# Optimization experiments

Measured on AMD Instinct MI355X. Metric: run time of the kernel, lower is better.

Reference implementation:

```python
import jax, jax.numpy as jnp
import numpy as np

BN_EPS = 1e-5


def conv1x1(x, w, b):
    # x: [B,C,H,W], w: [O,C] (squeezed 1x1 kernel), b: [O]
    return jnp.einsum('bchw,oc->bohw', x, w) + b[None, :, None, None]


def setup_inputs() -> dict:
    key = jax.random.key(0)
    ks = jax.random.split(key, 12)
    B, C, H, W = 4, 64, 256, 256
    s = 1.0 / np.sqrt(C).astype(np.float32)
    inp = {
        'x': jax.random.normal(ks[0], (B, C, H, W), jnp.float32),
        'theta_w': jax.random.normal(ks[1], (C, C), jnp.float32) * s,
        'theta_b': jax.random.normal(ks[2], (C,), jnp.float32) * 0.01,
        'phi_w': jax.random.normal(ks[3], (C, C), jnp.float32) * s,
        'phi_b': jax.random.normal(ks[4], (C,), jnp.float32) * 0.01,
        'g_w': jax.random.normal(ks[5], (C, C), jnp.float32) * s,
        'g_b': jax.random.normal(ks[6], (C,), jnp.float32) * 0.01,
        'w_w': jax.random.normal(ks[7], (C, C), jnp.float32) * s,
        'w_b': jax.random.normal(ks[8], (C,), jnp.float32) * 0.01,
        'bn_gamma': jax.random.normal(ks[9], (C,), jnp.float32) * 0.1,
        'bn_beta': jax.random.normal(ks[10], (C,), jnp.float32) * 0.1,
    }
    return inp


def reference(x, theta_w, theta_b, phi_w, phi_b, g_w, g_b, w_w, w_b, bn_gamma, bn_beta):
    B, C, H, W = x.shape
    N = H * W
    g_x = conv1x1(x, g_w, g_b).reshape(B, C, N)          # [B,C,N]
    theta_x = conv1x1(x, theta_w, theta_b).reshape(B, C, N)
    phi_x = conv1x1(x, phi_w, phi_b).reshape(B, C, N)
    # f = phi_x @ theta_x^T : channel-channel affinity [B,C,C]
    f = jnp.einsum('bcn,bdn->bcd', phi_x, theta_x)
    attn = jax.nn.softmax(f, axis=-1)                    # [B,C,C]
    y = jnp.einsum('bcd,bdn->bcn', attn, g_x)            # [B,C,N]
    # faithful to torch: permute(0,2,1).contiguous().view(B,C,H,W)
    y = jnp.transpose(y, (0, 2, 1)).reshape(B, C, H, W)
    w_y = conv1x1(y, w_w, w_b)                           # [B,C,H,W]
    # BatchNorm2d in training mode: batch stats over (B,H,W), biased var
    mean = jnp.mean(w_y, axis=(0, 2, 3), keepdims=True)
    var = jnp.var(w_y, axis=(0, 2, 3), keepdims=True)
    w_y = (w_y - mean) * jax.lax.rsqrt(var + BN_EPS)
    w_y = w_y * bn_gamma[None, :, None, None] + bn_beta[None, :, None, None]
    return w_y + x
```

## Files before the change

kernel.cpp:

```cpp
#include <hip/hip_runtime.h>
#include <hip/hip_bf16.h>
#include <stdint.h>

namespace {

constexpr size_t OFF_G     = 0;
constexpr size_t OFF_S     = 65536;
constexpr size_t OFF_M     = 66560;
constexpr size_t OFF_AB    = 132096;
constexpr size_t OFF_SCALE = 133120;
constexpr size_t OFF_STATS = 133632;
constexpr size_t OFF_WWT   = 134144;
constexpr size_t OFF_WSUM  = 150528;
constexpr size_t OFF_SPART = 150784;
constexpr size_t OFF_GPART = 412928;
constexpr size_t OFF_V     = 17190144;
constexpr size_t OFF_WY    = 50744576;

__device__ __forceinline__ float bf2f(unsigned short u) {
    return __uint_as_float(((unsigned)u) << 16);
}
__device__ __forceinline__ unsigned short f2bf(float f) {
    union { __hip_bfloat16 h; unsigned short u; } cv;
    cv.h = __float2bfloat16(f);
    return cv.u;
}

__global__ __launch_bounds__(256) void k_trans(const float* __restrict__ Ww,
                                               float* __restrict__ WwT,
                                               float* __restrict__ Wsum) {
    const int t = threadIdx.x;
    for (int e = t; e < 4096; e += 256) {
        const int o = e >> 6, c = e & 63;
        WwT[c * 64 + o] = Ww[e];
    }
    if (t < 64) {
        float s = 0.f;
#pragma unroll 8
        for (int c = 0; c < 64; ++c) s += Ww[t * 64 + c];
        Wsum[t] = s;
    }
}

__global__ __launch_bounds__(128) void k_gram(const float* __restrict__ x,
                                              float* __restrict__ gpart,
                                              float* __restrict__ spart) {
    const int wg = blockIdx.x;
    const int b = wg >> 8;
    const int chunk = wg & 255;
    const int t = threadIdx.x;
    const int wv = t >> 6;
    const int l = t & 63;
    const int g = l >> 3, h = l & 7;

    __shared__ __align__(16) float tile[64][64];
    __shared__ __align__(16) float Gred[4096];

    float acc[8][8];
#pragma unroll
    for (int i = 0; i < 8; ++i)
#pragma unroll
        for (int j = 0; j < 8; ++j) acc[i][j] = 0.f;
    float sp[8];
#pragma unroll
    for (int i = 0; i < 8; ++i) sp[i] = 0.f;

    const float* xb = x + (size_t)b * 64 * 65536 + chunk * 256;

    for (int t4 = 0; t4 < 4; ++t4) {
#pragma unroll
        for (int it = 0; it < 8; ++it) {
            const int v = it * 128 + t;
            const int row = v >> 4;
            const int c4 = v & 15;
            const float4 val = *(const float4*)(xb + (size_t)row * 65536 + t4 * 64 + c4 * 4);
            const int c4s = c4 ^ (row >> 3);
            *(float4*)&tile[row][c4s * 4] = val;
            sp[it] += val.x + val.y + val.z + val.w;
        }
        __syncthreads();
        const int fbase = wv * 8;
#pragma unroll
        for (int fs = 0; fs < 8; ++fs) {
            const int f = fbase + fs;
            float4 a4[8], b4[8];
#pragma unroll
            for (int i = 0; i < 8; ++i) a4[i] = *(const float4*)&tile[g * 8 + i][(f ^ g) * 4];
#pragma unroll
            for (int j = 0; j < 8; ++j) b4[j] = *(const float4*)&tile[h * 8 + j][(f ^ h) * 4];
#pragma unroll
            for (int i = 0; i < 8; ++i)
#pragma unroll
                for (int j = 0; j < 8; ++j) {
                    acc[i][j] += a4[i].x * b4[j].x;
                    acc[i][j] += a4[i].y * b4[j].y;
                    acc[i][j] += a4[i].z * b4[j].z;
                    acc[i][j] += a4[i].w * b4[j].w;
                }
        }
        __syncthreads();
    }

    if (wv == 1) {
#pragma unroll
        for (int i = 0; i < 8; ++i)
#pragma unroll
            for (int j4 = 0; j4 < 2; ++j4) {
                float4 v;
                v.x = acc[i][j4 * 4 + 0]; v.y = acc[i][j4 * 4 + 1];
                v.z = acc[i][j4 * 4 + 2]; v.w = acc[i][j4 * 4 + 3];
                *(float4*)&Gred[(g * 8 + i) * 64 + h * 8 + j4 * 4] = v;
            }
    }
    __syncthreads();
    if (wv == 0) {
        float* gp = gpart + (size_t)wg * 4096;
#pragma unroll
        for (int i = 0; i < 8; ++i)
#pragma unroll
            for (int j4 = 0; j4 < 2; ++j4) {
                const float4 r = *(const float4*)&Gred[(g * 8 + i) * 64 + h * 8 + j4 * 4];
                float4 v;
                v.x = acc[i][j4 * 4 + 0] + r.x; v.y = acc[i][j4 * 4 + 1] + r.y;
                v.z = acc[i][j4 * 4 + 2] + r.z; v.w = acc[i][j4 * 4 + 3] + r.w;
                *(float4*)(gp + (g * 8 + i) * 64 + h * 8 + j4 * 4) = v;
            }
    }
#pragma unroll
    for (int it = 0; it < 8; ++it) {
        float v = sp[it];
        v += __shfl_xor(v, 1);
        v += __shfl_xor(v, 2);
        v += __shfl_xor(v, 4);
        v += __shfl_xor(v, 8);
        if ((l & 15) == 0) {
            const int row = it * 8 + (t >> 4);
            spart[((size_t)b * 256 + chunk) * 64 + row] = v;
        }
    }
}

__global__ __launch_bounds__(256) void k_gred(const float* __restrict__ gpart,
                                              const float* __restrict__ spart,
                                              float* __restrict__ G,
                                              float* __restrict__ s) {
    const int b = blockIdx.x >> 4;
    const int part = blockIdx.x & 15;
    const int t = threadIdx.x;
    const int e4l = t & 63;
    const int cg = t >> 6;
    const int e4 = part * 64 + e4l;
    const float4* gp4 = (const float4*)gpart;

    float4 a = make_float4(0.f, 0.f, 0.f, 0.f);
#pragma unroll 8
    for (int i = 0; i < 64; ++i) {
        const int w = cg * 64 + i;
        const float4 v = gp4[((size_t)b * 256 + w) * 1024 + e4];
        a.x += v.x; a.y += v.y; a.z += v.z; a.w += v.w;
    }
    __shared__ __align__(16) float4 red[4][64];
    __shared__ float reds[4][64];
    red[cg][e4l] = a;

    float sv = 0.f;
    if (part == 0) {
#pragma unroll 8
        for (int i = 0; i < 64; ++i) {
            const int w = cg * 64 + i;
            sv += spart[((size_t)b * 256 + w) * 64 + e4l];
        }
        reds[cg][e4l] = sv;
    }
    __syncthreads();
    if (cg == 0) {
        const float4 r1 = red[1][e4l], r2 = red[2][e4l], r3 = red[3][e4l];
        float4 o;
        o.x = a.x + r1.x + r2.x + r3.x;
        o.y = a.y + r1.y + r2.y + r3.y;
        o.z = a.z + r1.z + r2.z + r3.z;
        o.w = a.w + r1.w + r2.w + r3.w;
        *(float4*)(G + (size_t)b * 4096 + (size_t)e4 * 4) = o;
        if (part == 0) {
            s[b * 64 + e4l] = sv + reds[1][e4l] + reds[2][e4l] + reds[3][e4l];
        }
    }
}

__global__ __launch_bounds__(256) void k_small(const float* __restrict__ G,
                                               const float* __restrict__ s,
                                               const float* __restrict__ Pw,
                                               const float* __restrict__ pb,
                                               const float* __restrict__ Tw,
                                               const float* __restrict__ tb,
                                               const float* __restrict__ Gw,
                                               const float* __restrict__ gb,
                                               float* __restrict__ M,
                                               float* __restrict__ ab) {
    const int b = blockIdx.x >> 1;
    const int rblk = (blockIdx.x & 1) * 32;
    const int t = threadIdx.x;
    const int rl = t >> 3;
    const int seg = t & 7;
    const int d0 = seg * 8;
    const int rg = rblk + rl;

    __shared__ __align__(16) float GL[64][68];
    __shared__ __align__(16) float TwL[64][68];
    __shared__ __align__(16) float GwL[64][68];
    __shared__ __align__(16) float PwL[32][68];
    __shared__ __align__(16) float AL[32][68];
    __shared__ __align__(16) float atL[32][68];
    __shared__ float sL[64], TsL[64], PsL[32], pbL[64], tbL[64], gbL[64];

    for (int v = t; v < 1024; v += 256) {
        const int k = v >> 4, c4 = (v & 15) * 4;
        *(float4*)&GL[k][c4]  = *(const float4*)(G + (size_t)b * 4096 + (size_t)v * 4);
        *(float4*)&TwL[k][c4] = *(const float4*)(Tw + (size_t)v * 4);
        *(float4*)&GwL[k][c4] = *(const float4*)(Gw + (size_t)v * 4);
    }
    for (int v = t; v < 512; v += 256) {
        const int k = v >> 4, c4 = (v & 15) * 4;
        *(float4*)&PwL[k][c4] = *(const float4*)(Pw + (size_t)(rblk + k) * 64 + c4);
    }
    if (t < 64) {
        sL[t] = s[b * 64 + t];
        pbL[t] = pb[t]; tbL[t] = tb[t]; gbL[t] = gb[t];
    }
    __syncthreads();
    if (t < 64) {
        float a = 0.f;
#pragma unroll 8
        for (int k = 0; k < 64; ++k) a += TwL[t][k] * sL[k];
        TsL[t] = a;
    }
    if (t < 32) {
        float a = 0.f;
#pragma unroll 8
        for (int k = 0; k < 64; ++k) a += PwL[t][k] * sL[k];
        PsL[t] = a;
    }
    {
        float4 a1 = make_float4(0.f, 0.f, 0.f, 0.f), a2 = make_float4(0.f, 0.f, 0.f, 0.f);
#pragma unroll 4
        for (int k = 0; k < 64; ++k) {
            const float pw = PwL[rl][k];
            const float4 g1 = *(const float4*)&GL[k][d0];
            const float4 g2 = *(const float4*)&GL[k][d0 + 4];
            a1.x += pw * g1.x; a1.y += pw * g1.y; a1.z += pw * g1.z; a1.w += pw * g1.w;
            a2.x += pw * g2.x; a2.y += pw * g2.y; a2.z += pw * g2.z; a2.w += pw * g2.w;
        }
        *(float4*)&AL[rl][d0] = a1;
        *(float4*)&AL[rl][d0 + 4] = a2;
    }
    __syncthreads();
    float4 areg[16];
#pragma unroll
    for (int i = 0; i < 16; ++i) areg[i] = *(const float4*)&AL[rl][i * 4];
    float fv[8];
#pragma unroll
    for (int dd = 0; dd < 8; ++dd) {
        const int d = d0 + dd;
        float4 a4 = make_float4(0.f, 0.f, 0.f, 0.f);
#pragma unroll
        for (int i = 0; i < 16; ++i) {
            const float4 tw = *(const float4*)&TwL[d][i * 4];
            a4.x += areg[i].x * tw.x; a4.y += areg[i].y * tw.y;
            a4.z += areg[i].z * tw.z; a4.w += areg[i].w * tw.w;
        }
        const float dot = (a4.x + a4.y) + (a4.z + a4.w);
        fv[dd] = dot + PsL[rl] * tbL[d] + pbL[rg] * (TsL[d] + 65536.f * tbL[d]);
    }
    float mx = fv[0];
#pragma unroll
    for (int dd = 1; dd < 8; ++dd) mx = fmaxf(mx, fv[dd]);
    mx = fmaxf(mx, __shfl_xor(mx, 1));
    mx = fmaxf(mx, __shfl_xor(mx, 2));
    mx = fmaxf(mx, __shfl_xor(mx, 4));
    float sm = 0.f;
#pragma unroll
    for (int dd = 0; dd < 8; ++dd) { fv[dd] = __expf(fv[dd] - mx); sm += fv[dd]; }
    sm += __shfl_xor(sm, 1);
    sm += __shfl_xor(sm, 2);
    sm += __shfl_xor(sm, 4);
    const float inv = 1.f / sm;
    float4 p1, p2;
    p1.x = fv[0] * inv; p1.y = fv[1] * inv; p1.z = fv[2] * inv; p1.w = fv[3] * inv;
    p2.x = fv[4] * inv; p2.y = fv[5] * inv; p2.z = fv[6] * inv; p2.w = fv[7] * inv;
    *(float4*)&atL[rl][d0] = p1;
    *(float4*)&atL[rl][d0 + 4] = p2;
    __syncthreads();
#pragma unroll
    for (int i = 0; i < 16; ++i) areg[i] = *(const float4*)&atL[rl][i * 4];
    float4 m1 = make_float4(0.f, 0.f, 0.f, 0.f), m2 = make_float4(0.f, 0.f, 0.f, 0.f);
    float abv = 0.f;
#pragma unroll
    for (int d4 = 0; d4 < 16; ++d4) {
        const float4 a = areg[d4];
#define MSTEP(comp, dc) { \
        const int d = d4 * 4 + dc; \
        const float ad = a.comp; \
        const float4 g1 = *(const float4*)&GwL[d][d0]; \
        const float4 g2 = *(const float4*)&GwL[d][d0 + 4]; \
        m1.x += ad * g1.x; m1.y += ad * g1.y; m1.z += ad * g1.z; m1.w += ad * g1.w; \
        m2.x += ad * g2.x; m2.y += ad * g2.y; m2.z += ad * g2.z; m2.w += ad * g2.w; \
        abv += ad * gbL[d]; }
        MSTEP(x, 0) MSTEP(y, 1) MSTEP(z, 2) MSTEP(w, 3)
#undef MSTEP
    }
    float* Mrow = M + ((size_t)b * 64 + rg) * 64;
    *(float4*)(Mrow + d0) = m1;
    *(float4*)(Mrow + d0 + 4) = m2;
    if (seg == 0) ab[b * 64 + rg] = abv;
}

__global__ __launch_bounds__(256) void k_convV(const float* __restrict__ x,
                                               const float* __restrict__ WwT,
                                               unsigned short* __restrict__ V) {
    const int bid = blockIdx.x;
    const int b = bid >> 8;
    const int k = (bid >> 2) & 63;
    const int qc = bid & 3;
    const int q = qc * 256 + threadIdx.x;
    const float* xr = x + ((size_t)b * 64 + k) * 65536 + q;
    float4 acc[16];
#pragma unroll
    for (int i = 0; i < 16; ++i) acc[i] = make_float4(0.f, 0.f, 0.f, 0.f);
#pragma unroll 2
    for (int cp = 0; cp < 64; ++cp) {
        const float xv = xr[(size_t)cp * 1024];
        const float4* wt = (const float4*)(WwT + cp * 64);
#pragma unroll
        for (int i = 0; i < 16; ++i) {
            const float4 w = wt[i];
            acc[i].x += w.x * xv; acc[i].y += w.y * xv;
            acc[i].z += w.z * xv; acc[i].w += w.w * xv;
        }
    }
    unsigned short* vp = V + (size_t)b * 64 * 65536 + (size_t)k * 1024 + q;
#pragma unroll
    for (int i = 0; i < 16; ++i) {
        vp[(size_t)(i * 4 + 0) * 65536] = f2bf(acc[i].x);
        vp[(size_t)(i * 4 + 1) * 65536] = f2bf(acc[i].y);
        vp[(size_t)(i * 4 + 2) * 65536] = f2bf(acc[i].z);
        vp[(size_t)(i * 4 + 3) * 65536] = f2bf(acc[i].w);
    }
}

__global__ __launch_bounds__(256) void k_wy(const unsigned short* __restrict__ V,
                                            const float* __restrict__ M,
                                            const float* __restrict__ ab,
                                            const float* __restrict__ Wsum,
                                            const float* __restrict__ wb,
                                            unsigned short* __restrict__ wy,
                                            float* __restrict__ stats) {
    const int bid = blockIdx.x;
    const int b = bid >> 9;
    const int o = (bid >> 3) & 63;
    const int qc = bid & 7;
    const int t = threadIdx.x;
    const int ql = t & 127;
    const int rh = __builtin_amdgcn_readfirstlane((t >> 7) * 32);
    const int q = qc * 128 + ql;

    const unsigned short* vsrc = V + ((size_t)b * 64 + o) * 65536 + q;
    float v[64];
#pragma unroll
    for (int k = 0; k < 64; ++k) v[k] = bf2f(vsrc[(size_t)k * 1024]);

    const float wsum_o = Wsum[o];
    const float wb_o = wb[o];
    const float* Mb = M + ((size_t)b * 64 + rh) * 64;
    const float* abb = ab + (size_t)b * 64 + rh;

    float ssum = 0.f, ssq = 0.f;
    unsigned pack[16];
#pragma unroll 4
    for (int ri = 0; ri < 32; ++ri) {
        const float4* mr4 = (const float4*)(Mb + ri * 64);
        float4 a4 = make_float4(0.f, 0.f, 0.f, 0.f);
#pragma unroll
        for (int i = 0; i < 16; ++i) {
            const float4 m = mr4[i];
            a4.x += m.x * v[i * 4 + 0];
            a4.y += m.y * v[i * 4 + 1];
            a4.z += m.z * v[i * 4 + 2];
            a4.w += m.w * v[i * 4 + 3];
        }
        const float val = (a4.x + a4.y) + (a4.z + a4.w) + wsum_o * abb[ri] + wb_o;
        ssum += val; ssq += val * val;
        const unsigned h = (unsigned)f2bf(val);
        if ((ri & 1) == 0) pack[ri >> 1] = h;
        else pack[ri >> 1] |= h << 16;
    }
    unsigned short* wp = wy + ((size_t)b * 64 + o) * 65536 + (size_t)q * 64 + rh;
#pragma unroll
    for (int i = 0; i < 4; ++i) {
        *(uint4*)(wp + i * 8) = make_uint4(pack[i * 4 + 0], pack[i * 4 + 1],
                                           pack[i * 4 + 2], pack[i * 4 + 3]);
    }
    float v1 = ssum, v2 = ssq;
#pragma unroll
    for (int off = 1; off < 64; off <<= 1) {
        v1 += __shfl_xor(v1, off);
        v2 += __shfl_xor(v2, off);
    }
    if ((t & 63) == 0) {
        atomicAdd(&stats[o], v1);
        atomicAdd(&stats[64 + o], v2);
    }
}

__global__ __launch_bounds__(64) void k_statfin(const float* __restrict__ stats,
                                                const float* __restrict__ gamma,
                                                const float* __restrict__ beta,
                                                float* __restrict__ scaleA,
                                                float* __restrict__ shiftB) {
    const int o = threadIdx.x;
    const float invn = 1.f / 262144.f;
    const float mean = stats[o] * invn;
    const float var = stats[64 + o] * invn - mean * mean;
    const float sA = gamma[o] * rsqrtf(var + 1e-5f);
    scaleA[o] = sA;
    shiftB[o] = beta[o] - mean * sA;
}

__global__ __launch_bounds__(256) void k_out(const unsigned short* __restrict__ wy,
                                             const float* __restrict__ x,
                                             const float* __restrict__ scaleA,
                                             const float* __restrict__ shiftB,
                                             float* __restrict__ out) {
    const size_t stride = (size_t)gridDim.x * blockDim.x;
    for (size_t i8 = (size_t)blockIdx.x * blockDim.x + threadIdx.x; i8 < 2097152; i8 += stride) {
        const size_t base = i8 * 8;
        const int o = (int)((base >> 16) & 63);
        const uint4 u = *(const uint4*)(wy + base);
        const float4 x1 = *(const float4*)(x + base);
        const float4 x2 = *(const float4*)(x + base + 4);
        const float a = scaleA[o];
        const float c = shiftB[o];
        float4 o1, o2;
        o1.x = __uint_as_float(u.x << 16) * a + c + x1.x;
        o1.y = __uint_as_float(u.x & 0xffff0000u) * a + c + x1.y;
        o1.z = __uint_as_float(u.y << 16) * a + c + x1.z;
        o1.w = __uint_as_float(u.y & 0xffff0000u) * a + c + x1.w;
        o2.x = __uint_as_float(u.z << 16) * a + c + x2.x;
        o2.y = __uint_as_float(u.z & 0xffff0000u) * a + c + x2.y;
        o2.z = __uint_as_float(u.w << 16) * a + c + x2.z;
        o2.w = __uint_as_float(u.w & 0xffff0000u) * a + c + x2.w;
        *(float4*)(out + base) = o1;
        *(float4*)(out + base + 4) = o2;
    }
}

}

extern "C" void kernel_launch(void* const* d_in, const int* in_sizes, int n_in,
                              void* d_out, int out_size, void* d_ws, size_t ws_size,
                              hipStream_t stream) {
    const float* x        = (const float*)d_in[0];
    const float* theta_w  = (const float*)d_in[1];
    const float* theta_b  = (const float*)d_in[2];
    const float* phi_w    = (const float*)d_in[3];
    const float* phi_b    = (const float*)d_in[4];
    const float* g_w      = (const float*)d_in[5];
    const float* g_b      = (const float*)d_in[6];
    const float* w_w      = (const float*)d_in[7];
    const float* w_b      = (const float*)d_in[8];
    const float* bn_gamma = (const float*)d_in[9];
    const float* bn_beta  = (const float*)d_in[10];
    float* out = (float*)d_out;
    char* ws = (char*)d_ws;

    float* G      = (float*)(ws + OFF_G);
    float* s      = (float*)(ws + OFF_S);
    float* M      = (float*)(ws + OFF_M);
    float* ab     = (float*)(ws + OFF_AB);
    float* scaleA = (float*)(ws + OFF_SCALE);
    float* shiftB = scaleA + 64;
    float* stats  = (float*)(ws + OFF_STATS);
    float* WwT    = (float*)(ws + OFF_WWT);
    float* Wsum   = (float*)(ws + OFF_WSUM);
    float* spart  = (float*)(ws + OFF_SPART);
    float* gpart  = (float*)(ws + OFF_GPART);
    unsigned short* V  = (unsigned short*)(ws + OFF_V);
    unsigned short* wy = (unsigned short*)(ws + OFF_WY);

    (void)in_sizes; (void)n_in; (void)out_size; (void)ws_size;

    hipMemsetAsync(stats, 0, 512, stream);
    hipLaunchKernelGGL(k_trans, dim3(1), dim3(256), 0, stream, w_w, WwT, Wsum);
    hipLaunchKernelGGL(k_gram, dim3(1024), dim3(128), 0, stream, x, gpart, spart);
    hipLaunchKernelGGL(k_gred, dim3(64), dim3(256), 0, stream, gpart, spart, G, s);
    hipLaunchKernelGGL(k_small, dim3(8), dim3(256), 0, stream, G, s, phi_w, phi_b,
                       theta_w, theta_b, g_w, g_b, M, ab);
    hipLaunchKernelGGL(k_convV, dim3(1024), dim3(256), 0, stream, x, WwT, V);
    hipLaunchKernelGGL(k_wy, dim3(2048), dim3(256), 0, stream, V, M, ab, Wsum, w_b, wy, stats);
    hipLaunchKernelGGL(k_statfin, dim3(1), dim3(64), 0, stream, stats, bn_gamma, bn_beta,
                       scaleA, shiftB);
    hipLaunchKernelGGL(k_out, dim3(2048), dim3(256), 0, stream, wy, x, scaleA, shiftB, out);
}
```

Measured before the change: 296.7 us.

## Register-tile convV and wy kernels as 16x8 outer products with vectorized bf16 I/O

Rewrites k_convV and k_wy so each thread computes a 16-output by 8-position register tile. Weights are broadcast per wave, and activations are loaded as float4/uint4 vectors instead of scalar strided loads. M is stored transposed so k_wy can read 16 contiguous rows per k. Output stores become packed 128-bit bf16 writes instead of scattered 16-bit stores. Grids halve or quarter and register pressure rises with 128 accumulators per thread, which may lower occupancy.

```diff
diff --git a/kernel.cpp b/kernel.cpp
--- a/kernel.cpp
+++ b/kernel.cpp
@@ -25,6 +25,9 @@
     cv.h = __float2bfloat16(f);
     return cv.u;
 }
+__device__ __forceinline__ unsigned pack2bf(float a, float b) {
+    return (unsigned)f2bf(a) | ((unsigned)f2bf(b) << 16);
+}
 
 __global__ __launch_bounds__(256) void k_trans(const float* __restrict__ Ww,
                                                float* __restrict__ WwT,
@@ -195,7 +198,7 @@
                                                const float* __restrict__ tb,
                                                const float* __restrict__ Gw,
                                                const float* __restrict__ gb,
-                                               float* __restrict__ M,
+                                               float* __restrict__ Mt,
                                                float* __restrict__ ab) {
     const int b = blockIdx.x >> 1;
     const int rblk = (blockIdx.x & 1) * 32;
@@ -308,9 +311,10 @@
         MSTEP(x, 0) MSTEP(y, 1) MSTEP(z, 2) MSTEP(w, 3)
 #undef MSTEP
     }
-    float* Mrow = M + ((size_t)b * 64 + rg) * 64;
-    *(float4*)(Mrow + d0) = m1;
-    *(float4*)(Mrow + d0 + 4) = m2;
+    float mv[8] = {m1.x, m1.y, m1.z, m1.w, m2.x, m2.y, m2.z, m2.w};
+    float* Mb = Mt + (size_t)b * 4096;
+#pragma unroll
+    for (int dd = 0; dd < 8; ++dd) Mb[(d0 + dd) * 64 + rg] = mv[dd];
     if (seg == 0) ab[b * 64 + rg] = abv;
 }
 
@@ -318,87 +322,134 @@
                                                const float* __restrict__ WwT,
                                                unsigned short* __restrict__ V) {
     const int bid = blockIdx.x;
-    const int b = bid >> 8;
-    const int k = (bid >> 2) & 63;
-    const int qc = bid & 3;
-    const int q = qc * 256 + threadIdx.x;
-    const float* xr = x + ((size_t)b * 64 + k) * 65536 + q;
-    float4 acc[16];
-#pragma unroll
-    for (int i = 0; i < 16; ++i) acc[i] = make_float4(0.f, 0.f, 0.f, 0.f);
-#pragma unroll 2
-    for (int cp = 0; cp < 64; ++cp) {
-        const float xv = xr[(size_t)cp * 1024];
-        const float4* wt = (const float4*)(WwT + cp * 64);
+    const int b = bid >> 7;
+    const int k = (bid >> 1) & 63;
+    const int qh = bid & 1;
+    const int t = threadIdx.x;
+    const int wv = __builtin_amdgcn_readfirstlane(t >> 6);
+    const int l = t & 63;
+    const int q0 = qh * 512 + l * 8;
+    const int o0 = wv * 16;
+
+    const float* xb = x + ((size_t)b * 64 + k) * 65536 + q0;
+    const float* wt = WwT + o0;
+
+    float acc[16][8];
+#pragma unroll
+    for (int i = 0; i < 16; ++i)
+#pragma unroll
+        for (int j = 0; j < 8; ++j) acc[i][j] = 0.f;
+
+    for (int c = 0; c < 64; ++c) {
+        const float4 x1 = *(const float4*)(xb + (size_t)c * 1024);
+        const float4 x2 = *(const float4*)(xb + (size_t)c * 1024 + 4);
+        const float xv[8] = {x1.x, x1.y, x1.z, x1.w, x2.x, x2.y, x2.z, x2.w};
+        const float4* wp = (const float4*)(wt + c * 64);
+        const float4 w0 = wp[0], w1 = wp[1], w2 = wp[2], w3 = wp[3];
+        const float wv16[16] = {w0.x, w0.y, w0.z, w0.w, w1.x, w1.y, w1.z, w1.w,
+                                w2.x, w2.y, w2.z, w2.w, w3.x, w3.y, w3.z, w3.w};
 #pragma unroll
         for (int i = 0; i < 16; ++i) {
-            const float4 w = wt[i];
-            acc[i].x += w.x * xv; acc[i].y += w.y * xv;
-            acc[i].z += w.z * xv; acc[i].w += w.w * xv;
-        }
-    }
-    unsigned short* vp = V + (size_t)b * 64 * 65536 + (size_t)k * 1024 + q;
+            const float w = wv16[i];
+#pragma unroll
+            for (int j = 0; j < 8; ++j) acc[i][j] += w * xv[j];
+        }
+    }
+    unsigned short* vb = V + (((size_t)b * 64 + o0) * 64 + k) * 1024 + q0;
 #pragma unroll
     for (int i = 0; i < 16; ++i) {
-        vp[(size_t)(i * 4 + 0) * 65536] = f2bf(acc[i].x);
-        vp[(size_t)(i * 4 + 1) * 65536] = f2bf(acc[i].y);
-        vp[(size_t)(i * 4 + 2) * 65536] = f2bf(acc[i].z);
-        vp[(size_t)(i * 4 + 3) * 65536] = f2bf(acc[i].w);
+        uint4 pk;
+        pk.x = pack2bf(acc[i][0], acc[i][1]);
+        pk.y = pack2bf(acc[i][2], acc[i][3]);
+        pk.z = pack2bf(acc[i][4], acc[i][5]);
+        pk.w = pack2bf(acc[i][6], acc[i][7]);
+        *(uint4*)(vb + (size_t)i * 65536) = pk;
     }
 }
 
 __global__ __launch_bounds__(256) void k_wy(const unsigned short* __restrict__ V,
-                                            const float* __restrict__ M,
+                                            const float* __restrict__ Mt,
                                             const float* __restrict__ ab,
                                             const float* __restrict__ Wsum,
                                             const float* __restrict__ wb,
                                             unsigned short* __restrict__ wy,
                                             float* __restrict__ stats) {
     const int bid = blockIdx.x;
-    const int b = bid >> 9;
-    const int o = (bid >> 3) & 63;
-    const int qc = bid & 7;
+    const int b = bid >> 7;
+    const int o = (bid >> 1) & 63;
+    const int qh = bid & 1;
     const int t = threadIdx.x;
-    const int ql = t & 127;
-    const int rh = __builtin_amdgcn_readfirstlane((t >> 7) * 32);
-    const int q = qc * 128 + ql;
-
-    const unsigned short* vsrc = V + ((size_t)b * 64 + o) * 65536 + q;
-    float v[64];
-#pragma unroll
-    for (int k = 0; k < 64; ++k) v[k] = bf2f(vsrc[(size_t)k * 1024]);
+    const int wv = __builtin_amdgcn_readfirstlane(t >> 6);
+    const int l = t & 63;
+    const int q0 = qh * 512 + l * 8;
+    const int r0 = wv * 16;
+
+    const unsigned short* vbase = V + ((size_t)b * 64 + o) * 65536 + q0;
+    const float* mt = Mt + (size_t)b * 4096 + r0;
+
+    float acc[16][8];
+#pragma unroll
+    for (int i = 0; i < 16; ++i)
+#pragma unroll
+        for (int j = 0; j < 8; ++j) acc[i][j] = 0.f;
+
+    for (int k = 0; k < 64; ++k) {
+        const uint4 u = *(const uint4*)(vbase + (size_t)k * 1024);
+        float v[8];
+        v[0] = __uint_as_float(u.x << 16);
+        v[1] = __uint_as_float(u.x & 0xffff0000u);
+        v[2] = __uint_as_float(u.y << 16);
+        v[3] = __uint_as_float(u.y & 0xffff0000u);
+        v[4] = __uint_as_float(u.z << 16);
+        v[5] = __uint_as_float(u.z & 0xffff0000u);
+        v[6] = __uint_as_float(u.w << 16);
+        v[7] = __uint_as_float(u.w & 0xffff0000u);
+        const float4* mp = (const float4*)(mt + k * 64);
+        const float4 m0 = mp[0], m1 = mp[1], m2 = mp[2], m3 = mp[3];
+        const float mv16[16] = {m0.x, m0.y, m0.z, m0.w, m1.x, m1.y, m1.z, m1.w,
+                                m2.x, m2.y, m2.z, m2.w, m3.x, m3.y, m3.z, m3.w};
+#pragma unroll
+        for (int i = 0; i < 16; ++i) {
+            const float m = mv16[i];
+#pragma unroll
+            for (int j = 0; j < 8; ++j) acc[i][j] += m * v[j];
+        }
+    }
 
     const float wsum_o = Wsum[o];
     const float wb_o = wb[o];
-    const float* Mb = M + ((size_t)b * 64 + rh) * 64;
-    const float* abb = ab + (size_t)b * 64 + rh;
+    const float* abb = ab + (size_t)b * 64 + r0;
+    float addv[16];
+#pragma unroll
+    for (int i = 0; i < 16; ++i) addv[i] = wsum_o * abb[i] + wb_o;
 
     float ssum = 0.f, ssq = 0.f;
-    unsigned pack[16];
-#pragma unroll 4
-    for (int ri = 0; ri < 32; ++ri) {
-        const float4* mr4 = (const float4*)(Mb + ri * 64);
-        float4 a4 = make_float4(0.f, 0.f, 0.f, 0.f);
-#pragma unroll
-        for (int i = 0; i < 16; ++i) {
-            const float4 m = mr4[i];
-            a4.x += m.x * v[i * 4 + 0];
-            a4.y += m.y * v[i * 4 + 1];
-            a4.z += m.z * v[i * 4 + 2];
-            a4.w += m.w * v[i * 4 + 3];
-        }
-        const float val = (a4.x + a4.y) + (a4.z + a4.w) + wsum_o * abb[ri] + wb_o;
-        ssum += val; ssq += val * val;
-        const unsigned h = (unsigned)f2bf(val);
-        if ((ri & 1) == 0) pack[ri >> 1] = h;
-        else pack[ri >> 1] |= h << 16;
-    }
-    unsigned short* wp = wy + ((size_t)b * 64 + o) * 65536 + (size_t)q * 64 + rh;
-#pragma unroll
-    for (int i = 0; i < 4; ++i) {
-        *(uint4*)(wp + i * 8) = make_uint4(pack[i * 4 + 0], pack[i * 4 + 1],
-                                           pack[i * 4 + 2], pack[i * 4 + 3]);
-    }
+#pragma unroll
+    for (int i = 0; i < 16; ++i)
+#pragma unroll
+        for (int j = 0; j < 8; ++j) {
+            const float val = acc[i][j] + addv[i];
+            acc[i][j] = val;
+            ssum += val;
+            ssq += val * val;
+        }
+
+    unsigned short* wyb = wy + ((size_t)b * 64 + o) * 65536 + (size_t)q0 * 64 + r0;
+#pragma unroll
+    for (int j = 0; j < 8; ++j) {
+        uint4 p1, p2;
+        p1.x = pack2bf(acc[0][j],  acc[1][j]);
+        p1.y = pack2bf(acc[2][j],  acc[3][j]);
+        p1.z = pack2bf(acc[4][j],  acc[5][j]);
+        p1.w = pack2bf(acc[6][j],  acc[7][j]);
+        p2.x = pack2bf(acc[8][j],  acc[9][j]);
+        p2.y = pack2bf(acc[10][j], acc[11][j]);
+        p2.z = pack2bf(acc[12][j], acc[13][j]);
+        p2.w = pack2bf(acc[14][j], acc[15][j]);
+        *(uint4*)(wyb + (size_t)j * 64) = p1;
+        *(uint4*)(wyb + (size_t)j * 64 + 8) = p2;
+    }
+
     float v1 = ssum, v2 = ssq;
 #pragma unroll
     for (int off = 1; off < 64; off <<= 1) {
@@ -474,7 +525,7 @@
 
     float* G      = (float*)(ws + OFF_G);
     float* s      = (float*)(ws + OFF_S);
-    float* M      = (float*)(ws + OFF_M);
+    float* Mt     = (float*)(ws + OFF_M);
     float* ab     = (float*)(ws + OFF_AB);
     float* scaleA = (float*)(ws + OFF_SCALE);
     float* shiftB = scaleA + 64;
@@ -493,9 +544,9 @@
     hipLaunchKernelGGL(k_gram, dim3(1024), dim3(128), 0, stream, x, gpart, spart);
     hipLaunchKernelGGL(k_gred, dim3(64), dim3(256), 0, stream, gpart, spart, G, s);
     hipLaunchKernelGGL(k_small, dim3(8), dim3(256), 0, stream, G, s, phi_w, phi_b,
-                       theta_w, theta_b, g_w, g_b, M, ab);
-    hipLaunchKernelGGL(k_convV, dim3(1024), dim3(256), 0, stream, x, WwT, V);
-    hipLaunchKernelGGL(k_wy, dim3(2048), dim3(256), 0, stream, V, M, ab, Wsum, w_b, wy, stats);
+                       theta_w, theta_b, g_w, g_b, Mt, ab);
+    hipLaunchKernelGGL(k_convV, dim3(512), dim3(256), 0, stream, x, WwT, V);
+    hipLaunchKernelGGL(k_wy, dim3(512), dim3(256), 0, stream, V, Mt, ab, Wsum, w_b, wy, stats);
     hipLaunchKernelGGL(k_statfin, dim3(1), dim3(64), 0, stream, stats, bn_gamma, bn_beta,
                        scaleA, shiftB);
     hipLaunchKernelGGL(k_out, dim3(2048), dim3(256), 0, stream, wy, x, scaleA, shiftB, out);
```

Measured after the change: 282.4 us. 1.05x faster.
